# Kernel tuning notes

Measured on AMD Instinct MI355X. Metric: run time of the kernel, lower is better.

Reference implementation:

```python
import jax, jax.numpy as jnp
import numpy as np

B, N, D = 2, 2048, 1024
H = 16
DH = D // H
WINDOW = 64
SCALE = 1.0 / np.sqrt(DH).astype(np.float32)


def setup_inputs() -> dict:
    key = jax.random.key(0)
    k1, k2, k3 = jax.random.split(key, 3)
    # xavier-uniform-like scales for the projections
    lim_qkv = np.sqrt(6.0 / (D + 3 * D)).astype(np.float32)
    lim_out = np.sqrt(6.0 / (D + D)).astype(np.float32)
    x = jax.random.normal(k1, (B, N, D), dtype=jnp.float32)
    Wqkv = jax.random.uniform(k2, (3 * D, D), dtype=jnp.float32, minval=-lim_qkv, maxval=lim_qkv)
    bqkv = jnp.zeros((3 * D,), dtype=jnp.float32)
    Wout = jax.random.uniform(k3, (D, D), dtype=jnp.float32, minval=-lim_out, maxval=lim_out)
    bout = jnp.zeros((D,), dtype=jnp.float32)
    return {"x": x, "Wqkv": Wqkv, "bqkv": bqkv, "Wout": Wout, "bout": bout}


def _causal_window_mask(n: int) -> jnp.ndarray:
    pos = jnp.arange(n)
    diff = pos[:, None] - pos[None, :]  # query_pos - key_pos
    return (diff >= 0) & (diff < WINDOW)  # [N, N] bool


def reference(x, Wqkv, bqkv, Wout, bout):
    b, n, d = x.shape
    qkv = x @ Wqkv.T + bqkv                      # [B, N, 3D]
    qkv = qkv.reshape(b, n, 3, H, DH)
    qkv = jnp.transpose(qkv, (2, 0, 3, 1, 4))    # [3, B, H, N, DH]
    q, k, v = qkv[0], qkv[1], qkv[2]
    scores = jnp.einsum('bhqd,bhkd->bhqk', q, k) * SCALE  # [B, H, N, N]
    mask = _causal_window_mask(n)
    neg_inf = jnp.asarray(-jnp.inf, dtype=scores.dtype)
    scores = jnp.where(mask[None, None], scores, neg_inf)
    attn = jax.nn.softmax(scores, axis=-1)
    out = jnp.einsum('bhqk,bhkd->bhqd', attn, v)  # [B, H, N, DH]
    out = jnp.transpose(out, (0, 2, 1, 3)).reshape(b, n, d)
    return out @ Wout.T + bout
```

## Files before the change

kernel.cpp:

```cpp
#include <hip/hip_runtime.h>
#include <hip/hip_bf16.h>


typedef __attribute__((ext_vector_type(8))) __bf16 bf16x8;
typedef __attribute__((ext_vector_type(4))) float f32x4;

#define GLOAD16(g, l)                                              \
  __builtin_amdgcn_global_load_lds(                                \
      (const __attribute__((address_space(1))) void*)(g),          \
      (__attribute__((address_space(3))) void*)(l), 16, 0, 0)

#define MFMA16(a, b, c) __builtin_amdgcn_mfma_f32_16x16x32_bf16((a), (b), (c), 0, 0, 0)

__global__ __launch_bounds__(256) void cvt3(const float* __restrict__ x,
                                            const float* __restrict__ wqkv,
                                            const float* __restrict__ wout,
                                            __bf16* __restrict__ xb,
                                            __bf16* __restrict__ wqkvb,
                                            __bf16* __restrict__ woutb) {
  const int blk = blockIdx.x;
  const float* src;
  __bf16* dst;
  int i;
  if (blk < 2048) {
    src = x; dst = xb; i = (blk * 256 + (int)threadIdx.x) * 8;
  } else if (blk < 3584) {
    src = wqkv; dst = wqkvb; i = ((blk - 2048) * 256 + (int)threadIdx.x) * 8;
  } else {
    src = wout; dst = woutb; i = ((blk - 3584) * 256 + (int)threadIdx.x) * 8;
  }
  f32x4 a = *(const f32x4*)(src + i);
  f32x4 b = *(const f32x4*)(src + i + 4);
  bf16x8 o;
  o[0] = (__bf16)a[0]; o[1] = (__bf16)a[1]; o[2] = (__bf16)a[2]; o[3] = (__bf16)a[3];
  o[4] = (__bf16)b[0]; o[5] = (__bf16)b[1]; o[6] = (__bf16)b[2]; o[7] = (__bf16)b[3];
  *(bf16x8*)(dst + i) = o;
}

template <int MODE>
__global__ __launch_bounds__(256) void gemm128(
    const __bf16* __restrict__ A, const __bf16* __restrict__ Bw,
    const float* __restrict__ bias, int M, int N, int K,
    float* __restrict__ outF,
    __bf16* __restrict__ qo, __bf16* __restrict__ ko, __bf16* __restrict__ vt) {
  __shared__ __align__(16) unsigned char As[128 * 256];
  __shared__ __align__(16) unsigned char Bs[128 * 256];
  const int tid = threadIdx.x;
  const int lane = tid & 63;
  const int wid = tid >> 6;
  const int wr = wid >> 1, wc = wid & 1;
  const int colL = lane & 15, g = lane >> 4;
  const int m0 = blockIdx.x * 128, n0 = blockIdx.y * 128;

  f32x4 acc[4][4] = {};

  const int nK = K >> 7;
  for (int ks = 0; ks < nK; ++ks) {
    const int k0 = ks << 7;
    __syncthreads();
#pragma unroll
    for (int it = 0; it < 8; ++it) {
      int c = tid + (it << 8);
      int row = c >> 4, p = c & 15;
      int q = p ^ (row & 7);
      GLOAD16(A + (size_t)(m0 + row) * K + (k0 + (q << 3)), As + c * 16);
      GLOAD16(Bw + (size_t)(n0 + row) * K + (k0 + (q << 3)), Bs + c * 16);
    }
    __syncthreads();
#pragma unroll
    for (int kk = 0; kk < 4; ++kk) {
      bf16x8 af[4], bf[4];
      const int slot = (kk << 2) + g;
#pragma unroll
      for (int mi = 0; mi < 4; ++mi) {
        int r = (wr << 6) + (mi << 4) + colL;
        af[mi] = *(const bf16x8*)(As + r * 256 + ((slot ^ (r & 7)) << 4));
      }
#pragma unroll
      for (int ni = 0; ni < 4; ++ni) {
        int r = (wc << 6) + (ni << 4) + colL;
        bf[ni] = *(const bf16x8*)(Bs + r * 256 + ((slot ^ (r & 7)) << 4));
      }
#pragma unroll
      for (int mi = 0; mi < 4; ++mi)
#pragma unroll
        for (int ni = 0; ni < 4; ++ni)
          acc[mi][ni] = MFMA16(af[mi], bf[ni], acc[mi][ni]);
    }
  }

#pragma unroll
  for (int ni = 0; ni < 4; ++ni) {
    const int Cn = n0 + (wc << 6) + (ni << 4) + colL;
    const float bv = bias[Cn];
    if (MODE == 0) {
      const int sx = Cn >> 10, h = (Cn >> 6) & 15, d = Cn & 63;
      const float mul = (sx == 0) ? 0.125f : 1.0f;
#pragma unroll
      for (int mi = 0; mi < 4; ++mi) {
#pragma unroll
        for (int j = 0; j < 4; ++j) {
          const int Rm = m0 + (wr << 6) + (mi << 4) + (g << 2) + j;
          const int bb = Rm >> 11, tt = Rm & 2047;
          const float v = (acc[mi][ni][j] + bv) * mul;
          if (sx == 2) {
            vt[(((size_t)bb * 16 + h) * 64 + d) * 2048 + tt] = (__bf16)v;
          } else {
            __bf16* dst = (sx == 0) ? qo : ko;
            dst[(((size_t)bb * 16 + h) * 2048 + tt) * 64 + d] = (__bf16)v;
          }
        }
      }
    } else {
#pragma unroll
      for (int mi = 0; mi < 4; ++mi) {
#pragma unroll
        for (int j = 0; j < 4; ++j) {
          const int Rm = m0 + (wr << 6) + (mi << 4) + (g << 2) + j;
          outF[(size_t)Rm * N + Cn] = acc[mi][ni][j] + bv;
        }
      }
    }
  }
}

__global__ __launch_bounds__(256) void attn_win(const __bf16* __restrict__ Qb,
                                                const __bf16* __restrict__ Kb,
                                                const __bf16* __restrict__ Vt,
                                                __bf16* __restrict__ Ob) {
  const int bh = blockIdx.x >> 5;
  const int qb = blockIdx.x & 31;
  const int b = bh >> 4, h = bh & 15;
  __shared__ __align__(16) unsigned char Qs[64 * 128];
  __shared__ __align__(16) unsigned char Ks[128 * 128];
  __shared__ __align__(16) unsigned char Vs[64 * 256];
  __shared__ __align__(16) unsigned char Ps[4 * 16 * 272];
  const int tid = threadIdx.x;
  const int lane = tid & 63;
  const int w = tid >> 6;
  const int colL = lane & 15, g = lane >> 4;
  const __bf16* Qg = Qb + (size_t)bh * 2048 * 64;
  const __bf16* Kg = Kb + (size_t)bh * 2048 * 64;
  const __bf16* Vg = Vt + (size_t)bh * 64 * 2048;
  const int t0 = qb * 64 - 64;

#pragma unroll
  for (int it = 0; it < 2; ++it) {
    int c = tid + (it << 8);
    int r = c >> 3, p = c & 7, q = p ^ (r & 7);
    GLOAD16(Qg + (size_t)(qb * 64 + r) * 64 + (q << 3), Qs + c * 16);
  }
#pragma unroll
  for (int it = 0; it < 4; ++it) {
    int c = tid + (it << 8);
    int r = c >> 3, p = c & 7, q = p ^ (r & 7);
    int tok = t0 + r;
    tok = tok < 0 ? 0 : tok;
    GLOAD16(Kg + (size_t)tok * 64 + (q << 3), Ks + c * 16);
  }
#pragma unroll
  for (int it = 0; it < 4; ++it) {
    int c = tid + (it << 8);
    int r = c >> 4, p = c & 15, q = p ^ (r & 7);
    int tk = t0 + (q << 3);
    tk = tk < 0 ? 0 : tk;
    GLOAD16(Vg + (size_t)r * 2048 + tk, Vs + c * 16);
  }
  __syncthreads();

  f32x4 sc[8] = {};
  bf16x8 qf[2];
#pragma unroll
  for (int kk = 0; kk < 2; ++kk) {
    int r = (w << 4) + colL;
    int slot = (kk << 2) + g;
    qf[kk] = *(const bf16x8*)(Qs + r * 128 + ((slot ^ (r & 7)) << 4));
  }
#pragma unroll
  for (int ni = 0; ni < 8; ++ni) {
#pragma unroll
    for (int kk = 0; kk < 2; ++kk) {
      int r = (ni << 4) + colL;
      int slot = (kk << 2) + g;
      bf16x8 kf = *(const bf16x8*)(Ks + r * 128 + ((slot ^ (r & 7)) << 4));
      sc[ni] = MFMA16(qf[kk], kf, sc[ni]);
    }
  }

  float mx[4], sm[4];
#pragma unroll
  for (int j = 0; j < 4; ++j) mx[j] = -3.0e38f;
#pragma unroll
  for (int ni = 0; ni < 8; ++ni) {
#pragma unroll
    for (int j = 0; j < 4; ++j) {
      const int qi = (w << 4) + (g << 2) + j;
      const int ki = (ni << 4) + colL;
      const bool valid = (ki > qi) && (ki <= qi + 64) && (qb > 0 || ki >= 64);
      if (!valid) sc[ni][j] = -3.0e38f;
      mx[j] = fmaxf(mx[j], sc[ni][j]);
    }
  }
#pragma unroll
  for (int j = 0; j < 4; ++j) {
    mx[j] = fmaxf(mx[j], __shfl_xor(mx[j], 1));
    mx[j] = fmaxf(mx[j], __shfl_xor(mx[j], 2));
    mx[j] = fmaxf(mx[j], __shfl_xor(mx[j], 4));
    mx[j] = fmaxf(mx[j], __shfl_xor(mx[j], 8));
    sm[j] = 0.0f;
  }
  unsigned char* ps = Ps + w * (16 * 272);
#pragma unroll
  for (int ni = 0; ni < 8; ++ni) {
#pragma unroll
    for (int j = 0; j < 4; ++j) {
      float p = __expf(sc[ni][j] - mx[j]);
      sm[j] += p;
      *(__bf16*)(ps + ((g << 2) + j) * 272 + (((ni << 4) + colL) << 1)) = (__bf16)p;
    }
  }
#pragma unroll
  for (int j = 0; j < 4; ++j) {
    sm[j] += __shfl_xor(sm[j], 1);
    sm[j] += __shfl_xor(sm[j], 2);
    sm[j] += __shfl_xor(sm[j], 4);
    sm[j] += __shfl_xor(sm[j], 8);
  }
  __syncthreads();

  f32x4 o[4] = {};
#pragma unroll
  for (int step = 0; step < 4; ++step) {
    bf16x8 pf = *(const bf16x8*)(ps + colL * 272 + (step << 6) + (g << 4));
#pragma unroll
    for (int dt = 0; dt < 4; ++dt) {
      int r = (dt << 4) + colL;
      int slot = (step << 2) + g;
      bf16x8 vf = *(const bf16x8*)(Vs + r * 256 + ((slot ^ (r & 7)) << 4));
      o[dt] = MFMA16(pf, vf, o[dt]);
    }
  }

  float rinv[4];
#pragma unroll
  for (int j = 0; j < 4; ++j) rinv[j] = 1.0f / sm[j];
#pragma unroll
  for (int dt = 0; dt < 4; ++dt) {
#pragma unroll
    for (int j = 0; j < 4; ++j) {
      const int t = qb * 64 + (w << 4) + (g << 2) + j;
      Ob[((size_t)b * 2048 + t) * 1024 + h * 64 + (dt << 4) + colL] =
          (__bf16)(o[dt][j] * rinv[j]);
    }
  }
}

extern "C" void kernel_launch(void* const* d_in, const int* in_sizes, int n_in,
                              void* d_out, int out_size, void* d_ws, size_t ws_size,
                              hipStream_t stream) {
  const float* x = (const float*)d_in[0];
  const float* Wqkv = (const float*)d_in[1];
  const float* bqkv = (const float*)d_in[2];
  const float* Wout = (const float*)d_in[3];
  const float* bout = (const float*)d_in[4];
  float* out = (float*)d_out;

  __bf16* xb = (__bf16*)d_ws;
  __bf16* Wqkvb = xb + 4194304;
  __bf16* Woutb = Wqkvb + 3145728;
  __bf16* Qb = Woutb + 1048576;
  __bf16* Kb = Qb + 4194304;
  __bf16* Vtb = Kb + 4194304;
  __bf16* AOb = Vtb + 4194304;

  cvt3<<<4096, 256, 0, stream>>>(x, Wqkv, Wout, xb, Wqkvb, Woutb);
  gemm128<0><<<dim3(32, 24), 256, 0, stream>>>(xb, Wqkvb, bqkv, 4096, 3072, 1024,
                                               nullptr, Qb, Kb, Vtb);
  attn_win<<<1024, 256, 0, stream>>>(Qb, Kb, Vtb, AOb);
  gemm128<1><<<dim3(32, 8), 256, 0, stream>>>(AOb, Woutb, bout, 4096, 1024, 1024,
                                              out, nullptr, nullptr, nullptr);
}
```

Before: 86.99 us.

## Replace QKV GEMM with 256x256 double-buffered pipelined kernel; shrink out-proj K tile

The QKV projection now uses a 256x256-tile, 512-thread kernel with double-buffered LDS and interleaved async global-to-LDS loads. Explicit vmcnt waits and barriers overlap memory transfer with MFMA work, setprio raises MFMA priority, and a block-index swizzle improves L2 locality. The output projection GEMM now uses a 64-wide K step, halving its LDS footprint, which may raise occupancy. The QKV grid drops to 192 blocks on a 256-CU part, so some CUs sit idle, and the hand-tuned wait counts are fragile.

```diff
diff --git a/kernel.cpp b/kernel.cpp
--- a/kernel.cpp
+++ b/kernel.cpp
@@ -37,14 +37,181 @@
   *(bf16x8*)(dst + i) = o;
 }
 
-template <int MODE>
-__global__ __launch_bounds__(256) void gemm128(
+
+#define BAR   __builtin_amdgcn_s_barrier()
+#define SBAR0 __builtin_amdgcn_sched_barrier(0)
+
+#define RD_AF(DST, ABASE, ALO)                                                     \
+  _Pragma("unroll")                                                                \
+  for (int a = 0; a < 4; ++a) {                                                    \
+    const int r = ((ALO) + a) * 16 + colL;                                         \
+    _Pragma("unroll")                                                              \
+    for (int kk = 0; kk < 2; ++kk)                                                 \
+      DST[a][kk] = *(const bf16x8*)((ABASE) + r * 128 +                            \
+                                    ((((kk << 2) + g) ^ (r & 7)) << 4));           \
+  }
+
+#define RD_BF(DST, BBASE, NLO)                                                     \
+  _Pragma("unroll")                                                                \
+  for (int nb = 0; nb < 2; ++nb) {                                                 \
+    const int r = ((wn & 1) << 6) + ((NLO) + nb) * 16 + colL;                      \
+    _Pragma("unroll")                                                              \
+    for (int kk = 0; kk < 2; ++kk)                                                 \
+      DST[nb][kk] = *(const bf16x8*)((BBASE) + r * 128 +                           \
+                                     ((((kk << 2) + g) ^ (r & 7)) << 4));          \
+  }
+
+#define QUADM(ALO, NLO, AF, BF)                                                    \
+  __builtin_amdgcn_s_setprio(1);                                                   \
+  _Pragma("unroll")                                                                \
+  for (int a = 0; a < 4; ++a)                                                      \
+    _Pragma("unroll")                                                              \
+    for (int nb = 0; nb < 2; ++nb) {                                               \
+      acc[(ALO) + a][(NLO) + nb] =                                                 \
+          MFMA16(AF[a][0], BF[nb][0], acc[(ALO) + a][(NLO) + nb]);                 \
+      acc[(ALO) + a][(NLO) + nb] =                                                 \
+          MFMA16(AF[a][1], BF[nb][1], acc[(ALO) + a][(NLO) + nb]);                 \
+    }                                                                              \
+  __builtin_amdgcn_s_setprio(0);
+
+__global__ __launch_bounds__(512, 2) void gemm256_qkv(
+    const __bf16* __restrict__ A, const __bf16* __restrict__ Bw,
+    const float* __restrict__ bias,
+    __bf16* __restrict__ qo, __bf16* __restrict__ ko, __bf16* __restrict__ vt) {
+  constexpr int K = 1024;
+  __shared__ __align__(16) unsigned char AsBuf[2][32768];
+  __shared__ __align__(16) unsigned char BsBuf[2][32768];
+  const int tid = threadIdx.x;
+  const int lane = tid & 63;
+  const int wid = tid >> 6;
+  const int wm = wid >> 2, wn = wid & 3;
+  const int colL = lane & 15, g = lane >> 4;
+
+  int s = blockIdx.x;
+  s = (s & 7) * 24 + (s >> 3);
+  const int m0 = (s / 12) * 256, n0 = (s % 12) * 256;
+
+  const __bf16* Ap0 = A + (size_t)m0 * K;
+  const __bf16* Ap1 = A + (size_t)(m0 + 128) * K;
+  const __bf16* Bp0 = Bw + (size_t)n0 * K;
+  const __bf16* Bp1 = Bw + (size_t)(n0 + 128) * K;
+
+  auto stage = [&](const __bf16* src, unsigned char* lds, int k0) {
+#pragma unroll
+    for (int it = 0; it < 2; ++it) {
+      int c = tid + (it << 9);
+      int row = c >> 3, pp = c & 7;
+      int q = pp ^ (row & 7);
+      GLOAD16(src + (size_t)row * K + k0 + (q << 3), lds + c * 16);
+    }
+  };
+
+  f32x4 acc[8][4] = {};
+
+  const unsigned char* A0b = AsBuf[0] + (wm << 14);
+  const unsigned char* A1b = AsBuf[1] + (wm << 14);
+  const unsigned char* B0b = BsBuf[0] + ((wn >> 1) << 14);
+  const unsigned char* B1b = BsBuf[1] + ((wn >> 1) << 14);
+
+  stage(Ap0, AsBuf[0], 0);
+  stage(Ap1, AsBuf[0] + 16384, 0);
+  stage(Bp0, BsBuf[0], 0);
+  stage(Bp1, BsBuf[0] + 16384, 0);
+  stage(Bp0, BsBuf[1], 64);
+  stage(Bp1, BsBuf[1] + 16384, 64);
+  stage(Ap0, AsBuf[1], 64);
+  asm volatile("s_waitcnt vmcnt(6)" ::: "memory");
+  BAR;
+
+  for (int i = 0; i < 8; ++i) {
+    const bool lst = (i == 7);
+    const int kc1 = (2 * i + 1) << 6;
+    const int kc2 = (2 * i + 2) << 6;
+    const int kc3 = (2 * i + 3) << 6;
+    bf16x8 afA[4][2], afB[4][2], bfA[2][2], bfB[2][2];
+
+    RD_AF(afA, A0b, 0);
+    RD_BF(bfA, B0b, 0);
+    stage(Ap1, AsBuf[1] + 16384, kc1);
+    SBAR0; BAR;
+    QUADM(0, 0, afA, bfA);
+    BAR;
+
+    RD_BF(bfB, B0b, 2);
+    SBAR0; BAR;
+    QUADM(0, 2, afA, bfB);
+    BAR;
+
+    RD_AF(afB, A0b, 4);
+    if (!lst) stage(Bp0, BsBuf[0], kc2);
+    SBAR0; BAR;
+    QUADM(4, 2, afB, bfB);
+    BAR;
+
+    if (!lst) stage(Bp1, BsBuf[0] + 16384, kc2);
+    SBAR0; BAR;
+    QUADM(4, 0, afB, bfA);
+    if (!lst) asm volatile("s_waitcnt vmcnt(4)" ::: "memory");
+    else      asm volatile("s_waitcnt vmcnt(0)" ::: "memory");
+    BAR;
+
+    RD_AF(afA, A1b, 0);
+    RD_BF(bfA, B1b, 0);
+    if (!lst) stage(Ap0, AsBuf[0], kc2);
+    SBAR0; BAR;
+    QUADM(0, 0, afA, bfA);
+    BAR;
+
+    RD_BF(bfB, B1b, 2);
+    if (!lst) stage(Ap1, AsBuf[0] + 16384, kc2);
+    SBAR0; BAR;
+    QUADM(0, 2, afA, bfB);
+    BAR;
+
+    RD_AF(afB, A1b, 4);
+    if (!lst) stage(Bp0, BsBuf[1], kc3);
+    SBAR0; BAR;
+    QUADM(4, 2, afB, bfB);
+    BAR;
+
+    if (!lst) { stage(Bp1, BsBuf[1] + 16384, kc3); stage(Ap0, AsBuf[1], kc3); }
+    SBAR0; BAR;
+    QUADM(4, 0, afB, bfA);
+    if (!lst) asm volatile("s_waitcnt vmcnt(6)" ::: "memory");
+    else      asm volatile("s_waitcnt vmcnt(0)" ::: "memory");
+    BAR;
+  }
+
+#pragma unroll
+  for (int ni = 0; ni < 4; ++ni) {
+    const int Cn = n0 + wn * 64 + ni * 16 + colL;
+    const float bv = bias[Cn];
+    const int sx = Cn >> 10, h = (Cn >> 6) & 15, d = Cn & 63;
+    const float mul = (sx == 0) ? 0.125f : 1.0f;
+#pragma unroll
+    for (int mi = 0; mi < 8; ++mi) {
+#pragma unroll
+      for (int j = 0; j < 4; ++j) {
+        const int Rm = m0 + wm * 128 + mi * 16 + (g << 2) + j;
+        const int bb = Rm >> 11, tt = Rm & 2047;
+        const float v = (acc[mi][ni][j] + bv) * mul;
+        if (sx == 2) {
+          vt[(((size_t)bb * 16 + h) * 64 + d) * 2048 + tt] = (__bf16)v;
+        } else {
+          __bf16* dst = (sx == 0) ? qo : ko;
+          dst[(((size_t)bb * 16 + h) * 2048 + tt) * 64 + d] = (__bf16)v;
+        }
+      }
+    }
+  }
+}
+
+__global__ __launch_bounds__(256) void gemm_bt_out(
     const __bf16* __restrict__ A, const __bf16* __restrict__ Bw,
     const float* __restrict__ bias, int M, int N, int K,
-    float* __restrict__ outF,
-    __bf16* __restrict__ qo, __bf16* __restrict__ ko, __bf16* __restrict__ vt) {
-  __shared__ __align__(16) unsigned char As[128 * 256];
-  __shared__ __align__(16) unsigned char Bs[128 * 256];
+    float* __restrict__ outF) {
+  __shared__ __align__(16) unsigned char As[128 * 128];
+  __shared__ __align__(16) unsigned char Bs[128 * 128];
   const int tid = threadIdx.x;
   const int lane = tid & 63;
   const int wid = tid >> 6;
@@ -54,32 +221,32 @@
 
   f32x4 acc[4][4] = {};
 
-  const int nK = K >> 7;
+  const int nK = K >> 6;
   for (int ks = 0; ks < nK; ++ks) {
-    const int k0 = ks << 7;
+    const int k0 = ks << 6;
     __syncthreads();
 #pragma unroll
-    for (int it = 0; it < 8; ++it) {
+    for (int it = 0; it < 4; ++it) {
       int c = tid + (it << 8);
-      int row = c >> 4, p = c & 15;
+      int row = c >> 3, p = c & 7;
       int q = p ^ (row & 7);
       GLOAD16(A + (size_t)(m0 + row) * K + (k0 + (q << 3)), As + c * 16);
       GLOAD16(Bw + (size_t)(n0 + row) * K + (k0 + (q << 3)), Bs + c * 16);
     }
     __syncthreads();
 #pragma unroll
-    for (int kk = 0; kk < 4; ++kk) {
+    for (int kk = 0; kk < 2; ++kk) {
       bf16x8 af[4], bf[4];
       const int slot = (kk << 2) + g;
 #pragma unroll
       for (int mi = 0; mi < 4; ++mi) {
         int r = (wr << 6) + (mi << 4) + colL;
-        af[mi] = *(const bf16x8*)(As + r * 256 + ((slot ^ (r & 7)) << 4));
+        af[mi] = *(const bf16x8*)(As + r * 128 + ((slot ^ (r & 7)) << 4));
       }
 #pragma unroll
       for (int ni = 0; ni < 4; ++ni) {
         int r = (wc << 6) + (ni << 4) + colL;
-        bf[ni] = *(const bf16x8*)(Bs + r * 256 + ((slot ^ (r & 7)) << 4));
+        bf[ni] = *(const bf16x8*)(Bs + r * 128 + ((slot ^ (r & 7)) << 4));
       }
 #pragma unroll
       for (int mi = 0; mi < 4; ++mi)
@@ -93,32 +260,12 @@
   for (int ni = 0; ni < 4; ++ni) {
     const int Cn = n0 + (wc << 6) + (ni << 4) + colL;
     const float bv = bias[Cn];
-    if (MODE == 0) {
-      const int sx = Cn >> 10, h = (Cn >> 6) & 15, d = Cn & 63;
-      const float mul = (sx == 0) ? 0.125f : 1.0f;
-#pragma unroll
-      for (int mi = 0; mi < 4; ++mi) {
-#pragma unroll
-        for (int j = 0; j < 4; ++j) {
-          const int Rm = m0 + (wr << 6) + (mi << 4) + (g << 2) + j;
-          const int bb = Rm >> 11, tt = Rm & 2047;
-          const float v = (acc[mi][ni][j] + bv) * mul;
-          if (sx == 2) {
-            vt[(((size_t)bb * 16 + h) * 64 + d) * 2048 + tt] = (__bf16)v;
-          } else {
-            __bf16* dst = (sx == 0) ? qo : ko;
-            dst[(((size_t)bb * 16 + h) * 2048 + tt) * 64 + d] = (__bf16)v;
-          }
-        }
-      }
-    } else {
-#pragma unroll
-      for (int mi = 0; mi < 4; ++mi) {
-#pragma unroll
-        for (int j = 0; j < 4; ++j) {
-          const int Rm = m0 + (wr << 6) + (mi << 4) + (g << 2) + j;
-          outF[(size_t)Rm * N + Cn] = acc[mi][ni][j] + bv;
-        }
+#pragma unroll
+    for (int mi = 0; mi < 4; ++mi) {
+#pragma unroll
+      for (int j = 0; j < 4; ++j) {
+        const int Rm = m0 + (wr << 6) + (mi << 4) + (g << 2) + j;
+        outF[(size_t)Rm * N + Cn] = acc[mi][ni][j] + bv;
       }
     }
   }
@@ -274,9 +421,7 @@
   __bf16* AOb = Vtb + 4194304;
 
   cvt3<<<4096, 256, 0, stream>>>(x, Wqkv, Wout, xb, Wqkvb, Woutb);
-  gemm128<0><<<dim3(32, 24), 256, 0, stream>>>(xb, Wqkvb, bqkv, 4096, 3072, 1024,
-                                               nullptr, Qb, Kb, Vtb);
+  gemm256_qkv<<<192, 512, 0, stream>>>(xb, Wqkvb, bqkv, Qb, Kb, Vtb);
   attn_win<<<1024, 256, 0, stream>>>(Qb, Kb, Vtb, AOb);
-  gemm128<1><<<dim3(32, 8), 256, 0, stream>>>(AOb, Woutb, bout, 4096, 1024, 1024,
-                                              out, nullptr, nullptr, nullptr);
+  gemm_bt_out<<<dim3(32, 8), 256, 0, stream>>>(AOb, Woutb, bout, 4096, 1024, 1024, out);
 }
```

New measurement: 110.5 us. 27.0% more time.

## Double-buffer GEMM K-tiles, remap blocks across XCDs, move V transpose to separate kernel

Applied to the files above, without the earlier changes.

Rewrites the GEMM to use 32-wide K tiles in two LDS buffers, so global loads for tile t+2 are in flight while MFMAs run on tile t. This replaces the single 128-wide K stage that stalled on a full load each iteration. Block indices are remapped in chunks, apparently so neighbouring tiles land on the same XCD and share L2. The strided transposed V store in the QKV epilogue becomes a plain row-major store, and a separate LDS-based transpose kernel produces Vt, at the cost of an extra launch and an extra pass over V.

```diff
diff --git a/kernel.cpp b/kernel.cpp
--- a/kernel.cpp
+++ b/kernel.cpp
@@ -38,55 +38,80 @@
 }
 
 template <int MODE>
-__global__ __launch_bounds__(256) void gemm128(
+__global__ __launch_bounds__(256) void gemm_db(
     const __bf16* __restrict__ A, const __bf16* __restrict__ Bw,
     const float* __restrict__ bias, int M, int N, int K,
     float* __restrict__ outF,
-    __bf16* __restrict__ qo, __bf16* __restrict__ ko, __bf16* __restrict__ vt) {
-  __shared__ __align__(16) unsigned char As[128 * 256];
-  __shared__ __align__(16) unsigned char Bs[128 * 256];
+    __bf16* __restrict__ qo, __bf16* __restrict__ ko, __bf16* __restrict__ vo,
+    int nbn, int chunk) {
+  __shared__ __align__(16) unsigned char Ls[32768];
   const int tid = threadIdx.x;
   const int lane = tid & 63;
   const int wid = tid >> 6;
   const int wr = wid >> 1, wc = wid & 1;
   const int colL = lane & 15, g = lane >> 4;
-  const int m0 = blockIdx.x * 128, n0 = blockIdx.y * 128;
+
+  int s = (int)blockIdx.x;
+  s = (s & 7) * chunk + (s >> 3);
+  const int m0 = (s / nbn) * 128, n0 = (s % nbn) * 128;
+
+  const __bf16* Ap = A + (size_t)m0 * K;
+  const __bf16* Bp = Bw + (size_t)n0 * K;
+
+  auto stage2 = [&](const __bf16* src, unsigned char* lds, int k0) {
+#pragma unroll
+    for (int it = 0; it < 2; ++it) {
+      int c = tid + (it << 8);
+      int L = c >> 3, s6 = c & 7;
+      int u = s6 ^ (L & 7);
+      int row = (L << 1) | (u >> 2), p = u & 3;
+      GLOAD16(src + (size_t)row * K + k0 + (p << 3), lds + c * 16);
+    }
+  };
 
   f32x4 acc[4][4] = {};
 
-  const int nK = K >> 7;
-  for (int ks = 0; ks < nK; ++ks) {
-    const int k0 = ks << 7;
-    __syncthreads();
-#pragma unroll
-    for (int it = 0; it < 8; ++it) {
-      int c = tid + (it << 8);
-      int row = c >> 4, p = c & 15;
-      int q = p ^ (row & 7);
-      GLOAD16(A + (size_t)(m0 + row) * K + (k0 + (q << 3)), As + c * 16);
-      GLOAD16(Bw + (size_t)(n0 + row) * K + (k0 + (q << 3)), Bs + c * 16);
-    }
-    __syncthreads();
-#pragma unroll
-    for (int kk = 0; kk < 4; ++kk) {
-      bf16x8 af[4], bf[4];
-      const int slot = (kk << 2) + g;
-#pragma unroll
-      for (int mi = 0; mi < 4; ++mi) {
-        int r = (wr << 6) + (mi << 4) + colL;
-        af[mi] = *(const bf16x8*)(As + r * 256 + ((slot ^ (r & 7)) << 4));
-      }
-#pragma unroll
-      for (int ni = 0; ni < 4; ++ni) {
-        int r = (wc << 6) + (ni << 4) + colL;
-        bf[ni] = *(const bf16x8*)(Bs + r * 256 + ((slot ^ (r & 7)) << 4));
-      }
-#pragma unroll
-      for (int mi = 0; mi < 4; ++mi)
-#pragma unroll
-        for (int ni = 0; ni < 4; ++ni)
-          acc[mi][ni] = MFMA16(af[mi], bf[ni], acc[mi][ni]);
-    }
+  stage2(Ap, Ls, 0);
+  stage2(Bp, Ls + 8192, 0);
+  stage2(Ap, Ls + 16384, 32);
+  stage2(Bp, Ls + 24576, 32);
+  asm volatile("s_waitcnt vmcnt(4)" ::: "memory");
+  __builtin_amdgcn_s_barrier();
+
+  const int nT = K >> 5;
+  for (int t = 0; t < nT; ++t) {
+    const unsigned char* Ab = Ls + (t & 1) * 16384;
+    const unsigned char* Bb = Ab + 8192;
+    bf16x8 af[4], bf[4];
+#pragma unroll
+    for (int mi = 0; mi < 4; ++mi) {
+      const int r = (wr << 6) + (mi << 4) + colL;
+      af[mi] = *(const bf16x8*)(Ab + (r >> 1) * 128 +
+                                (((((r & 1) << 2) | g) ^ ((r >> 1) & 7)) << 4));
+    }
+#pragma unroll
+    for (int ni = 0; ni < 4; ++ni) {
+      const int r = (wc << 6) + (ni << 4) + colL;
+      bf[ni] = *(const bf16x8*)(Bb + (r >> 1) * 128 +
+                                (((((r & 1) << 2) | g) ^ ((r >> 1) & 7)) << 4));
+    }
+#pragma unroll
+    for (int mi = 0; mi < 4; ++mi)
+#pragma unroll
+      for (int ni = 0; ni < 4; ++ni)
+        acc[mi][ni] = MFMA16(af[mi], bf[ni], acc[mi][ni]);
+    asm volatile("s_waitcnt lgkmcnt(0)" ::: "memory");
+    __builtin_amdgcn_s_barrier();
+    if (t < nT - 2) {
+      const int kn = (t + 2) << 5;
+      unsigned char* dst = Ls + (t & 1) * 16384;
+      stage2(Ap, dst, kn);
+      stage2(Bp, dst + 8192, kn);
+      asm volatile("s_waitcnt vmcnt(4)" ::: "memory");
+    } else {
+      asm volatile("s_waitcnt vmcnt(0)" ::: "memory");
+    }
+    __builtin_amdgcn_s_barrier();
   }
 
 #pragma unroll
@@ -95,6 +120,7 @@
     const float bv = bias[Cn];
     if (MODE == 0) {
       const int sx = Cn >> 10, h = (Cn >> 6) & 15, d = Cn & 63;
+      __bf16* dst = (sx == 0) ? qo : (sx == 1 ? ko : vo);
       const float mul = (sx == 0) ? 0.125f : 1.0f;
 #pragma unroll
       for (int mi = 0; mi < 4; ++mi) {
@@ -102,13 +128,8 @@
         for (int j = 0; j < 4; ++j) {
           const int Rm = m0 + (wr << 6) + (mi << 4) + (g << 2) + j;
           const int bb = Rm >> 11, tt = Rm & 2047;
-          const float v = (acc[mi][ni][j] + bv) * mul;
-          if (sx == 2) {
-            vt[(((size_t)bb * 16 + h) * 64 + d) * 2048 + tt] = (__bf16)v;
-          } else {
-            __bf16* dst = (sx == 0) ? qo : ko;
-            dst[(((size_t)bb * 16 + h) * 2048 + tt) * 64 + d] = (__bf16)v;
-          }
+          dst[(((size_t)bb * 16 + h) * 2048 + tt) * 64 + d] =
+              (__bf16)((acc[mi][ni][j] + bv) * mul);
         }
       }
     } else {
@@ -121,6 +142,33 @@
         }
       }
     }
+  }
+}
+
+__global__ __launch_bounds__(256) void transpose_v(const __bf16* __restrict__ Vb,
+                                                   __bf16* __restrict__ Vt) {
+  const int blk = blockIdx.x;
+  const int bh = blk >> 5;
+  const int t0 = (blk & 31) << 6;
+  __shared__ __align__(16) __bf16 ts[64][72];
+  const int tid = threadIdx.x;
+  const __bf16* src = Vb + ((size_t)bh * 2048 + t0) * 64;
+#pragma unroll
+  for (int it = 0; it < 2; ++it) {
+    int c = tid + (it << 8);
+    int r = c >> 3, q8 = (c & 7) << 3;
+    *(bf16x8*)&ts[r][q8] = *(const bf16x8*)(src + r * 64 + q8);
+  }
+  __syncthreads();
+  __bf16* dst = Vt + (size_t)bh * 64 * 2048 + t0;
+#pragma unroll
+  for (int it = 0; it < 2; ++it) {
+    int c = tid + (it << 8);
+    int d = c >> 3, j8 = (c & 7) << 3;
+    bf16x8 o;
+#pragma unroll
+    for (int e = 0; e < 8; ++e) o[e] = ts[j8 + e][d];
+    *(bf16x8*)(dst + (size_t)d * 2048 + j8) = o;
   }
 }
 
@@ -270,13 +318,15 @@
   __bf16* Woutb = Wqkvb + 3145728;
   __bf16* Qb = Woutb + 1048576;
   __bf16* Kb = Qb + 4194304;
-  __bf16* Vtb = Kb + 4194304;
+  __bf16* Vb = Kb + 4194304;
+  __bf16* Vtb = Vb + 4194304;
   __bf16* AOb = Vtb + 4194304;
 
   cvt3<<<4096, 256, 0, stream>>>(x, Wqkv, Wout, xb, Wqkvb, Woutb);
-  gemm128<0><<<dim3(32, 24), 256, 0, stream>>>(xb, Wqkvb, bqkv, 4096, 3072, 1024,
-                                               nullptr, Qb, Kb, Vtb);
+  gemm_db<0><<<768, 256, 0, stream>>>(xb, Wqkvb, bqkv, 4096, 3072, 1024,
+                                      nullptr, Qb, Kb, Vb, 24, 96);
+  transpose_v<<<1024, 256, 0, stream>>>(Vb, Vtb);
   attn_win<<<1024, 256, 0, stream>>>(Qb, Kb, Vtb, AOb);
-  gemm128<1><<<dim3(32, 8), 256, 0, stream>>>(AOb, Woutb, bout, 4096, 1024, 1024,
-                                              out, nullptr, nullptr, nullptr);
-}
+  gemm_db<1><<<256, 256, 0, stream>>>(AOb, Woutb, bout, 4096, 1024, 1024,
+                                      out, nullptr, nullptr, nullptr, 8, 32);
+}
```

Result: slower. 90.42 us (+3.9%).

## Double-buffer GEMM K loop, remap blocks for L2 locality, transpose V via LDS

Applied to the files above, without the earlier changes.

Replaces the single-buffered 128-K GEMM with a double-buffered 64-K pipeline that issues the next tile's global-to-LDS loads while MFMAs run on the current one, using explicit vmcnt waits and raw barriers. Blocks are remapped with an XCD-aware chunked swizzle for cache locality. The output projection uses 64x128 tiles with 128 threads to get more blocks. The V transpose epilogue is staged through LDS so stores become coalesced 4-byte writes instead of scattered 2-byte stores. Hand-written waitcnt counts and the block remap add risk of ordering errors and depend on the fixed grid sizes.

```diff
diff --git a/kernel.cpp b/kernel.cpp
--- a/kernel.cpp
+++ b/kernel.cpp
@@ -37,88 +37,162 @@
   *(bf16x8*)(dst + i) = o;
 }
 
-template <int MODE>
-__global__ __launch_bounds__(256) void gemm128(
+template <int MODE, int WM>
+__global__ __launch_bounds__(WM * 128) void gemm_ct(
     const __bf16* __restrict__ A, const __bf16* __restrict__ Bw,
-    const float* __restrict__ bias, int M, int N, int K,
+    const float* __restrict__ bias, int N,
     float* __restrict__ outF,
-    __bf16* __restrict__ qo, __bf16* __restrict__ ko, __bf16* __restrict__ vt) {
-  __shared__ __align__(16) unsigned char As[128 * 256];
-  __shared__ __align__(16) unsigned char Bs[128 * 256];
+    __bf16* __restrict__ qo, __bf16* __restrict__ ko, __bf16* __restrict__ vt,
+    int nbn, int chunk) {
+  constexpr int K = 1024;
+  constexpr int ASZ = WM * 8192;
+  constexpr int BUF = ASZ + 16384;
+  __shared__ __align__(16) unsigned char Ls[2 * BUF];
   const int tid = threadIdx.x;
   const int lane = tid & 63;
   const int wid = tid >> 6;
-  const int wr = wid >> 1, wc = wid & 1;
+  const int wr = (WM == 2) ? (wid >> 1) : 0;
+  const int wc = (WM == 2) ? (wid & 1) : wid;
   const int colL = lane & 15, g = lane >> 4;
-  const int m0 = blockIdx.x * 128, n0 = blockIdx.y * 128;
+
+  int s = (int)blockIdx.x;
+  s = (s & 7) * chunk + (s >> 3);
+  const int m0 = (s / nbn) * (WM * 64), n0 = (s % nbn) * 128;
+
+  const __bf16* Ap = A + (size_t)m0 * K;
+  const __bf16* Bp = Bw + (size_t)n0 * K;
+
+  auto stageA = [&](unsigned char* lds, int k0) {
+#pragma unroll
+    for (int it = 0; it < 4; ++it) {
+      int c = tid + it * (WM * 128);
+      int row = c >> 3, p = c & 7, q = p ^ (row & 7);
+      GLOAD16(Ap + (size_t)row * K + k0 + (q << 3), lds + c * 16);
+    }
+  };
+  auto stageB = [&](unsigned char* lds, int k0) {
+#pragma unroll
+    for (int it = 0; it < 8 / WM; ++it) {
+      int c = tid + it * (WM * 128);
+      int row = c >> 3, p = c & 7, q = p ^ (row & 7);
+      GLOAD16(Bp + (size_t)row * K + k0 + (q << 3), lds + c * 16);
+    }
+  };
 
   f32x4 acc[4][4] = {};
 
-  const int nK = K >> 7;
-  for (int ks = 0; ks < nK; ++ks) {
-    const int k0 = ks << 7;
-    __syncthreads();
-#pragma unroll
-    for (int it = 0; it < 8; ++it) {
-      int c = tid + (it << 8);
-      int row = c >> 4, p = c & 15;
-      int q = p ^ (row & 7);
-      GLOAD16(A + (size_t)(m0 + row) * K + (k0 + (q << 3)), As + c * 16);
-      GLOAD16(Bw + (size_t)(n0 + row) * K + (k0 + (q << 3)), Bs + c * 16);
-    }
-    __syncthreads();
-#pragma unroll
-    for (int kk = 0; kk < 4; ++kk) {
-      bf16x8 af[4], bf[4];
-      const int slot = (kk << 2) + g;
-#pragma unroll
-      for (int mi = 0; mi < 4; ++mi) {
-        int r = (wr << 6) + (mi << 4) + colL;
-        af[mi] = *(const bf16x8*)(As + r * 256 + ((slot ^ (r & 7)) << 4));
+  stageA(Ls, 0);
+  stageB(Ls + ASZ, 0);
+  stageA(Ls + BUF, 64);
+  stageB(Ls + BUF + ASZ, 64);
+  if constexpr (WM == 2) asm volatile("s_waitcnt vmcnt(8)" ::: "memory");
+  else                   asm volatile("s_waitcnt vmcnt(12)" ::: "memory");
+  __builtin_amdgcn_s_barrier();
+
+  constexpr int nT = 16;
+  for (int t = 0; t < nT; ++t) {
+    const unsigned char* Ab = Ls + (t & 1) * BUF;
+    const unsigned char* Bb = Ab + ASZ;
+    bf16x8 af[4][2], bf[4][2];
+#pragma unroll
+    for (int mi = 0; mi < 4; ++mi) {
+      const int r = (wr << 6) + (mi << 4) + colL;
+#pragma unroll
+      for (int kk = 0; kk < 2; ++kk)
+        af[mi][kk] = *(const bf16x8*)(Ab + r * 128 + ((((kk << 2) + g) ^ (r & 7)) << 4));
+    }
+#pragma unroll
+    for (int ni = 0; ni < 4; ++ni) {
+      const int r = (wc << 6) + (ni << 4) + colL;
+#pragma unroll
+      for (int kk = 0; kk < 2; ++kk)
+        bf[ni][kk] = *(const bf16x8*)(Bb + r * 128 + ((((kk << 2) + g) ^ (r & 7)) << 4));
+    }
+#pragma unroll
+    for (int mi = 0; mi < 4; ++mi)
+#pragma unroll
+      for (int ni = 0; ni < 4; ++ni) {
+        acc[mi][ni] = MFMA16(af[mi][0], bf[ni][0], acc[mi][ni]);
+        acc[mi][ni] = MFMA16(af[mi][1], bf[ni][1], acc[mi][ni]);
       }
-#pragma unroll
-      for (int ni = 0; ni < 4; ++ni) {
-        int r = (wc << 6) + (ni << 4) + colL;
-        bf[ni] = *(const bf16x8*)(Bs + r * 256 + ((slot ^ (r & 7)) << 4));
+    asm volatile("s_waitcnt lgkmcnt(0)" ::: "memory");
+    __builtin_amdgcn_s_barrier();
+    if (t < nT - 2) {
+      const int kn = (t + 2) << 6;
+      unsigned char* dst = Ls + (t & 1) * BUF;
+      stageA(dst, kn);
+      stageB(dst + ASZ, kn);
+      if constexpr (WM == 2) asm volatile("s_waitcnt vmcnt(8)" ::: "memory");
+      else                   asm volatile("s_waitcnt vmcnt(12)" ::: "memory");
+    } else {
+      asm volatile("s_waitcnt vmcnt(0)" ::: "memory");
+    }
+    __builtin_amdgcn_s_barrier();
+  }
+
+  if (MODE == 0) {
+    const int Cn0 = n0 + (wc << 6);
+    const int sx = Cn0 >> 10, h = (Cn0 >> 6) & 15;
+    float bv[4];
+#pragma unroll
+    for (int ni = 0; ni < 4; ++ni) bv[ni] = bias[Cn0 + (ni << 4) + colL];
+    const int b = m0 >> 11;
+    if (sx == 2) {
+      unsigned char* wreg = Ls + wid * 9216;
+#pragma unroll
+      for (int mi = 0; mi < 4; ++mi)
+#pragma unroll
+        for (int ni = 0; ni < 4; ++ni)
+#pragma unroll
+          for (int jp = 0; jp < 2; ++jp) {
+            const int tt = (mi << 4) + (g << 2) + (jp << 1);
+            const int d = (ni << 4) + colL;
+            unsigned short u0 = __builtin_bit_cast(
+                unsigned short, (__bf16)(acc[mi][ni][jp * 2] + bv[ni]));
+            unsigned short u1 = __builtin_bit_cast(
+                unsigned short, (__bf16)(acc[mi][ni][jp * 2 + 1] + bv[ni]));
+            *(unsigned int*)(wreg + ((d * 72 + tt) << 1)) =
+                (unsigned int)u0 | ((unsigned int)u1 << 16);
+          }
+      asm volatile("s_waitcnt lgkmcnt(0)" ::: "memory");
+      const size_t vbase = (size_t)(b * 16 + h) * 64 * 2048;
+      const int tg0 = (m0 & 2047) + (wr << 6);
+#pragma unroll
+      for (int i = 0; i < 32; ++i) {
+        const int d = (i << 1) + (lane >> 5);
+        const int toff = (lane & 31) << 1;
+        unsigned int v = *(unsigned int*)(wreg + (d * 144 + ((lane & 31) << 2)));
+        *(unsigned int*)((unsigned short*)vt + vbase + (size_t)d * 2048 + tg0 + toff) = v;
       }
-#pragma unroll
-      for (int mi = 0; mi < 4; ++mi)
-#pragma unroll
-        for (int ni = 0; ni < 4; ++ni)
-          acc[mi][ni] = MFMA16(af[mi], bf[ni], acc[mi][ni]);
-    }
-  }
-
-#pragma unroll
-  for (int ni = 0; ni < 4; ++ni) {
-    const int Cn = n0 + (wc << 6) + (ni << 4) + colL;
-    const float bv = bias[Cn];
-    if (MODE == 0) {
-      const int sx = Cn >> 10, h = (Cn >> 6) & 15, d = Cn & 63;
+    } else {
+      __bf16* dst = (sx == 0) ? qo : ko;
       const float mul = (sx == 0) ? 0.125f : 1.0f;
 #pragma unroll
       for (int mi = 0; mi < 4; ++mi) {
 #pragma unroll
         for (int j = 0; j < 4; ++j) {
           const int Rm = m0 + (wr << 6) + (mi << 4) + (g << 2) + j;
-          const int bb = Rm >> 11, tt = Rm & 2047;
-          const float v = (acc[mi][ni][j] + bv) * mul;
-          if (sx == 2) {
-            vt[(((size_t)bb * 16 + h) * 64 + d) * 2048 + tt] = (__bf16)v;
-          } else {
-            __bf16* dst = (sx == 0) ? qo : ko;
-            dst[(((size_t)bb * 16 + h) * 2048 + tt) * 64 + d] = (__bf16)v;
-          }
+          const int tt = Rm & 2047;
+          __bf16* rowp = dst + (((size_t)b * 16 + h) * 2048 + tt) * 64;
+#pragma unroll
+          for (int ni = 0; ni < 4; ++ni)
+            rowp[(ni << 4) + colL] = (__bf16)((acc[mi][ni][j] + bv[ni]) * mul);
         }
       }
-    } else {
-#pragma unroll
-      for (int mi = 0; mi < 4; ++mi) {
-#pragma unroll
-        for (int j = 0; j < 4; ++j) {
-          const int Rm = m0 + (wr << 6) + (mi << 4) + (g << 2) + j;
-          outF[(size_t)Rm * N + Cn] = acc[mi][ni][j] + bv;
-        }
+    }
+  } else {
+    float bv[4];
+#pragma unroll
+    for (int ni = 0; ni < 4; ++ni) bv[ni] = bias[n0 + (wc << 6) + (ni << 4) + colL];
+#pragma unroll
+    for (int mi = 0; mi < 4; ++mi) {
+#pragma unroll
+      for (int j = 0; j < 4; ++j) {
+        const int Rm = m0 + (wr << 6) + (mi << 4) + (g << 2) + j;
+        float* rowp = outF + (size_t)Rm * N + n0 + (wc << 6);
+#pragma unroll
+        for (int ni = 0; ni < 4; ++ni)
+          rowp[(ni << 4) + colL] = acc[mi][ni][j] + bv[ni];
       }
     }
   }
@@ -274,9 +348,9 @@
   __bf16* AOb = Vtb + 4194304;
 
   cvt3<<<4096, 256, 0, stream>>>(x, Wqkv, Wout, xb, Wqkvb, Woutb);
-  gemm128<0><<<dim3(32, 24), 256, 0, stream>>>(xb, Wqkvb, bqkv, 4096, 3072, 1024,
-                                               nullptr, Qb, Kb, Vtb);
+  gemm_ct<0, 2><<<768, 256, 0, stream>>>(xb, Wqkvb, bqkv, 3072, nullptr,
+                                         Qb, Kb, Vtb, 24, 96);
   attn_win<<<1024, 256, 0, stream>>>(Qb, Kb, Vtb, AOb);
-  gemm128<1><<<dim3(32, 8), 256, 0, stream>>>(AOb, Woutb, bout, 4096, 1024, 1024,
-                                              out, nullptr, nullptr, nullptr);
+  gemm_ct<1, 1><<<512, 128, 0, stream>>>(AOb, Woutb, bout, 1024, out,
+                                         nullptr, nullptr, nullptr, 8, 64);
 }
```

New measurement: 72.87 us. 16.2% less time.
